# Performance work log

Measured on AMD Instinct MI355X. Metric: run time of the kernel, lower is better.

Reference implementation:

```python
import jax, jax.numpy as jnp
import numpy as np

N_EMB = 512
EMB_DIM = 64
DECAY = 0.99
EPS = 1e-5


def setup_inputs() -> dict:
    key = jax.random.key(0)
    k1, k2 = jax.random.split(key)
    x = jax.random.normal(k1, (32, EMB_DIM, 64, 64), dtype=jnp.float32)
    weight = jax.random.uniform(k2, (EMB_DIM, N_EMB), dtype=jnp.float32)  # rd_init=True: torch.rand(emb_dim, n_emb)
    cluster_size = jnp.zeros((N_EMB,), dtype=jnp.float32)
    embed_avg = weight  # buffer initialized as embed.clone()
    return {"x": x, "weight": weight, "cluster_size": cluster_size, "embed_avg": embed_avg}


def reference(x, weight, cluster_size, embed_avg):
    B, D, H, W = x.shape
    n_emb = weight.shape[1]
    # (B, D, H, W) -> (N, D) tokens
    flat = jnp.transpose(x, (0, 2, 3, 1)).reshape(-1, D)
    dist = (jnp.sum(flat * flat, axis=1, keepdims=True)
            - 2.0 * (flat @ weight)
            + jnp.sum(weight * weight, axis=0)[None, :])
    argmin = jnp.argmin(dist, axis=1)                      # (N,)
    quant = jnp.take(weight.T, argmin, axis=0)             # gather -> (N, D)
    result = jnp.transpose(quant.reshape(B, H, W, D), (0, 3, 1, 2))  # (B, D, H, W)

    # --- EMA codebook update (training branch) ---
    ones = jnp.ones(argmin.shape, dtype=x.dtype)
    n_idx = jax.ops.segment_sum(ones, argmin, num_segments=n_emb)    # onehot.sum(0)
    n_idx = jnp.where(n_idx == 0, jnp.ones_like(n_idx), n_idx)       # clamp empty clusters to 1
    new_cluster_size = DECAY * cluster_size + (1.0 - DECAY) * n_idx
    embed_sum = jax.ops.segment_sum(flat, argmin, num_segments=n_emb).T  # flatten.T @ onehot -> (D, n_emb)
    new_embed_avg = DECAY * embed_avg + (1.0 - DECAY) * embed_sum
    n = jnp.sum(new_cluster_size)
    cs = (new_cluster_size + EPS) / (n + n_emb * EPS) * n
    new_weight = new_embed_avg / cs[None, :]

    return result, argmin.reshape(B, H, W), new_weight, new_cluster_size, new_embed_avg
```

## Files before the change

kernel.cpp:

```cpp
#include <hip/hip_runtime.h>

#define NEMB 512
#define EMB 64
#define BSTR 262144
#define DECAYF 0.99f
#define OMDF 0.01f
#define EPSF 1e-5f
#define GAP_T 4e-4f
#define QCAP 32768

typedef __attribute__((ext_vector_type(8))) short bf16x8;
typedef __attribute__((ext_vector_type(4))) float f32x4;

__device__ __forceinline__ unsigned short f2bf(float f) {
    unsigned u = __float_as_uint(f);
    return (unsigned short)((u + 0x7FFFu + ((u >> 16) & 1u)) >> 16);
}
__device__ __forceinline__ float bf2f(unsigned short h) {
    return __uint_as_float(((unsigned)h) << 16);
}

__device__ __forceinline__ void gl2lds16(const void* g, void* l) {
    __builtin_amdgcn_global_load_lds(
        (const __attribute__((address_space(1))) unsigned int*)g,
        (__attribute__((address_space(3))) unsigned int*)l, 16, 0, 0);
}

__global__ void prep_kernel(const float* __restrict__ w,
                            unsigned short* __restrict__ wh, unsigned short* __restrict__ wl,
                            float* __restrict__ wsq,
                            float* __restrict__ cnt_ws, unsigned* __restrict__ gcnt) {
    int j = threadIdx.x;
    if (blockIdx.x < 8) {
        int d0 = blockIdx.x << 3;
        bf16x8 hb, lb;
#pragma unroll
        for (int i = 0; i < 8; ++i) {
            float v = w[(d0 + i) * NEMB + j];
            unsigned short h = f2bf(v);
            hb[i] = (short)h;
            lb[i] = (short)f2bf(v - bf2f(h));
        }
        *(bf16x8*)(wh + j * EMB + d0) = hb;
        *(bf16x8*)(wl + j * EMB + d0) = lb;
    } else {
        float s = 0.f;
#pragma unroll
        for (int d = 0; d < EMB; ++d) { float v = w[d * NEMB + j]; s = fmaf(v, v, s); }
        wsq[j] = s;
        cnt_ws[j] = 0.f;
        if (j == 0) *gcnt = 0u;
    }
}

#define UPD(S1, J1, S2, J2, s_, j_) do { \
    if (s_ < S1 || (s_ == S1 && j_ < J1)) { S2 = S1; J2 = J1; S1 = s_; J1 = j_; } \
    else if (s_ < S2 || (s_ == S2 && j_ < J2)) { S2 = s_; J2 = j_; } } while (0)

__global__ __launch_bounds__(512, 4) void vq_main(
    const float* __restrict__ x,
    const unsigned short* __restrict__ wh, const unsigned short* __restrict__ wl,
    const float* __restrict__ wsq,
    float* __restrict__ out_arg, unsigned* __restrict__ gcnt, int* __restrict__ queue)
{
    __shared__ __align__(16) unsigned char ubuf[32768];
    __shared__ float wsq_s[NEMB];

    float* xt = (float*)ubuf;
    unsigned short* whq = (unsigned short*)ubuf;
    unsigned short* wlq = whq + 8192;

    const int tid = threadIdx.x;
    const int blk = blockIdx.x;
    const int b    = blk >> 5;
    const int hgrp = blk & 31;
    const int t0 = b * 4096 + hgrp * 128;
    const float* xbase = x + b * BSTR + hgrp * 128;

    const int lane = tid & 63;
    const int wave = tid >> 6;

#pragma unroll
    for (int it = 0; it < 4; ++it) {
        int ch = wave + (it << 3);
        int d0 = ch << 1;
        gl2lds16(xbase + (d0 + (lane >> 5)) * 4096 + ((lane & 31) << 2),
                 xt + d0 * 128);
    }
    wsq_s[tid] = wsq[tid];
    __syncthreads();

    const int l15  = lane & 15;
    const int quad = lane >> 4;
    const int wbase = wave << 4;

    bf16x8 ah[2], al[2];
    float xq[4];
    {
        int m = wbase + l15;
        float sq = 0.f;
#pragma unroll
        for (int ks = 0; ks < 2; ++ks) {
            int k0 = (ks << 5) + (quad << 3);
            bf16x8 hh, ll;
#pragma unroll
            for (int i = 0; i < 8; ++i) {
                float v = xt[(k0 + i) * 128 + m];
                sq = fmaf(v, v, sq);
                unsigned short h = f2bf(v);
                hh[i] = (short)h;
                ll[i] = (short)f2bf(v - bf2f(h));
            }
            ah[ks] = hh; al[ks] = ll;
        }
        sq += __shfl_xor(sq, 16, 64);
        sq += __shfl_xor(sq, 32, 64);
#pragma unroll
        for (int r = 0; r < 4; ++r)
            xq[r] = __shfl(sq, (quad << 2) + r, 64);
    }
    __syncthreads();

    float v1[4], v2[4];
    int   j1[4];
#pragma unroll
    for (int r = 0; r < 4; ++r) { v1[r] = 3.4e38f; v2[r] = 3.4e38f; j1[r] = 0; }

    const int m7 = l15 & 7;
    const int s0off = ((quad ^ m7) << 3);
    const int s1off = (((4 | quad) ^ m7) << 3);

#pragma unroll
    for (int it = 0; it < 4; ++it) {
        int g0 = (wave << 6) + (it << 9);
        int arr = g0 >> 10;
        int win0 = g0 & 1023;
        int win = win0 + lane;
        int row = win >> 3, slot = win & 7;
        const unsigned short* src =
            (arr ? wl : wh) + row * EMB + ((slot ^ (row & 7)) << 3);
        gl2lds16(src, (arr ? wlq : whq) + (win0 << 3));
    }
    __syncthreads();

    for (int q = 0; q < 4; ++q) {
        const int nbase = q << 7;
#pragma unroll 2
        for (int it = 0; it < 8; ++it) {
            const int ib = ((it << 4) + l15) << 6;
            bf16x8 b0 = *(const bf16x8*)(whq + ib + s0off);
            bf16x8 b1 = *(const bf16x8*)(whq + ib + s1off);
            bf16x8 b2 = *(const bf16x8*)(wlq + ib + s0off);
            bf16x8 b3 = *(const bf16x8*)(wlq + ib + s1off);
            const int n = nbase + (it << 4) + l15;
            float wq = wsq_s[n];

            f32x4 acc = (f32x4){0.f, 0.f, 0.f, 0.f};
            acc = __builtin_amdgcn_mfma_f32_16x16x32_bf16(ah[0], b0, acc, 0, 0, 0);
            acc = __builtin_amdgcn_mfma_f32_16x16x32_bf16(ah[1], b1, acc, 0, 0, 0);
            acc = __builtin_amdgcn_mfma_f32_16x16x32_bf16(ah[0], b2, acc, 0, 0, 0);
            acc = __builtin_amdgcn_mfma_f32_16x16x32_bf16(ah[1], b3, acc, 0, 0, 0);
            acc = __builtin_amdgcn_mfma_f32_16x16x32_bf16(al[0], b0, acc, 0, 0, 0);
            acc = __builtin_amdgcn_mfma_f32_16x16x32_bf16(al[1], b1, acc, 0, 0, 0);
            acc = __builtin_amdgcn_mfma_f32_16x16x32_bf16(al[0], b2, acc, 0, 0, 0);
            acc = __builtin_amdgcn_mfma_f32_16x16x32_bf16(al[1], b3, acc, 0, 0, 0);

#pragma unroll
            for (int r = 0; r < 4; ++r) {
                float s0 = fmaf(-2.f, acc[r], xq[r] + wq);
                bool p0 = s0 < v1[r];
                float mx0 = fmaxf(s0, v1[r]);
                v1[r] = fminf(s0, v1[r]);
                v2[r] = fminf(v2[r], mx0);
                j1[r] = p0 ? n : j1[r];
            }
        }
        if (q < 3) {
            __syncthreads();
#pragma unroll
            for (int it = 0; it < 4; ++it) {
                int g0 = (wave << 6) + (it << 9);
                int arr = g0 >> 10;
                int win0 = g0 & 1023;
                int win = win0 + lane;
                int row = win >> 3, slot = win & 7;
                const unsigned short* src =
                    (arr ? wl : wh) + (((q + 1) << 7) + row) * EMB + ((slot ^ (row & 7)) << 3);
                gl2lds16(src, (arr ? wlq : whq) + (win0 << 3));
            }
            __syncthreads();
        }
    }

#pragma unroll
    for (int r = 0; r < 4; ++r) {
        float a1 = v1[r], a2 = v2[r];
        int   aj = j1[r];
#pragma unroll
        for (int msk = 1; msk < 16; msk <<= 1) {
            float o1 = __shfl_xor(a1, msk, 64);
            int   oj = __shfl_xor(aj, msk, 64);
            float o2 = __shfl_xor(a2, msk, 64);
            bool take = (o1 < a1) || (o1 == a1 && oj < aj);
            float mx = fmaxf(a1, o1);
            a2 = fminf(fminf(a2, o2), mx);
            a1 = fminf(a1, o1);
            aj = take ? oj : aj;
        }
        v1[r] = a1; v2[r] = a2; j1[r] = aj;
    }

    if (l15 == 0) {
#pragma unroll
        for (int r = 0; r < 4; ++r) {
            int gt = t0 + wbase + (quad << 2) + r;
            out_arg[gt] = (float)j1[r];
            if (v2[r] - v1[r] < GAP_T) {
                unsigned idx = atomicAdd(gcnt, 1u);
                if (idx < QCAP) queue[idx] = gt;
            }
        }
    }
}

__global__ __launch_bounds__(256) void refine_kernel(
    const float* __restrict__ x, const float* __restrict__ w,
    const float* __restrict__ wsq, const unsigned* __restrict__ gcnt,
    const int* __restrict__ queue, float* __restrict__ out_arg)
{
    __shared__ float wsq_s[NEMB];
    const int tid = threadIdx.x;
    wsq_s[tid] = wsq[tid];
    wsq_s[tid + 256] = wsq[tid + 256];
    __syncthreads();

    unsigned nfu = *gcnt;
    const int nf = (int)(nfu < (unsigned)QCAP ? nfu : (unsigned)QCAP);
    const int lane = tid & 63;
    const int gw = (blockIdx.x << 2) + (tid >> 6);

    for (int i = gw; i < nf; i += 1024) {
        const int t = queue[i] & 131071;
        const int b = t >> 12, pos = t & 4095;
        float xd = x[b * BSTR + lane * 4096 + pos];
        float xqv = xd * xd;
#pragma unroll
        for (int mk = 1; mk < 64; mk <<= 1) xqv += __shfl_xor(xqv, mk, 64);

        float accv[8];
#pragma unroll
        for (int k = 0; k < 8; ++k) accv[k] = 0.f;
#pragma unroll 4
        for (int d = 0; d < EMB; ++d) {
            float4 wa = *(const float4*)(w + d * NEMB + (lane << 2));
            float4 wb = *(const float4*)(w + d * NEMB + 256 + (lane << 2));
            float xv = __shfl(xd, d, 64);
            accv[0] = fmaf(xv, wa.x, accv[0]);
            accv[1] = fmaf(xv, wa.y, accv[1]);
            accv[2] = fmaf(xv, wa.z, accv[2]);
            accv[3] = fmaf(xv, wa.w, accv[3]);
            accv[4] = fmaf(xv, wb.x, accv[4]);
            accv[5] = fmaf(xv, wb.y, accv[5]);
            accv[6] = fmaf(xv, wb.z, accv[6]);
            accv[7] = fmaf(xv, wb.w, accv[7]);
        }

        float S1 = 3.4e38f, S2 = 3.4e38f; int J1 = 0, J2 = 0;
#pragma unroll
        for (int k = 0; k < 8; ++k) {
            int j = (k < 4) ? ((lane << 2) + k) : (256 + (lane << 2) + k - 4);
            float s = (xqv - 2.f * accv[k]) + wsq_s[j];
            UPD(S1, J1, S2, J2, s, j);
        }
#pragma unroll
        for (int mk = 1; mk < 64; mk <<= 1) {
            float os1 = __shfl_xor(S1, mk, 64); int oj1 = __shfl_xor(J1, mk, 64);
            float os2 = __shfl_xor(S2, mk, 64); int oj2 = __shfl_xor(J2, mk, 64);
            UPD(S1, J1, S2, J2, os1, oj1);
            UPD(S1, J1, S2, J2, os2, oj2);
        }

        int jm = J1;
        if (S2 - S1 < 1e-3f) {
            float w1 = w[lane * NEMB + J1];
            float w2 = w[lane * NEMB + J2];
            double e1 = (double)w1 * (double)w1 - 2.0 * (double)xd * (double)w1;
            double e2 = (double)w2 * (double)w2 - 2.0 * (double)xd * (double)w2;
#pragma unroll
            for (int mk = 1; mk < 64; mk <<= 1) {
                e1 += __shfl_xor(e1, mk, 64);
                e2 += __shfl_xor(e2, mk, 64);
            }
            if (e2 < e1 || (e2 == e1 && J2 < J1)) jm = J2;
        }
        if (lane == 0) out_arg[t] = (float)jm;
    }
}

__global__ __launch_bounds__(512, 4) void es_kernel(
    const float* __restrict__ x, const float* __restrict__ arg,
    float* __restrict__ es_p, float* __restrict__ cnt_ws)
{
    __shared__ unsigned short xh[16384];
    __shared__ int args_s[256];
    __shared__ float cacc[NEMB];

    const int tid = threadIdx.x;
    const int blk = blockIdx.x;
    const int flavor = blk & 1;
    const int chunk  = blk >> 1;
    const int b = chunk >> 3;
    const int tpos0 = (chunk & 7) << 9;

    cacc[tid] = 0.f;

    const int lane = tid & 63;
    const int wave = tid >> 6;
    const int l15  = lane & 15;
    const int quad = lane >> 4;
    const int jb   = wave << 5;

    f32x4 acc[4][2];
#pragma unroll
    for (int m = 0; m < 4; ++m)
#pragma unroll
        for (int nc = 0; nc < 2; ++nc) acc[m][nc] = (f32x4){0.f, 0.f, 0.f, 0.f};

    for (int st = 0; st < 2; ++st) {
        const int tpos = tpos0 + (st << 8);
#pragma unroll
        for (int it = 0; it < 8; ++it) {
            int idx = tid + (it << 9);
            int d = idx >> 6, q = idx & 63;
            float4 g = *(const float4*)(x + b * BSTR + d * 4096 + tpos + (q << 2));
            int c = q >> 1, half = q & 1;
            int off = d * 256 + ((c ^ (d & 7)) << 3) + (half << 2);
            ushort4 hv = {f2bf(g.x), f2bf(g.y), f2bf(g.z), f2bf(g.w)};
            *(ushort4*)(xh + off) = hv;
        }
        if (tid < 256) args_s[tid] = ((int)arg[b * 4096 + tpos + tid]) & 511;
        __syncthreads();

        if (flavor == 0 && tid < 256) atomicAdd(&cacc[args_s[tid]], 1.f);

#pragma unroll
        for (int kk = 0; kk < 8; ++kk) {
            bf16x8 a_[4];
#pragma unroll
            for (int m = 0; m < 4; ++m) {
                int d = (m << 4) + l15;
                int coff = ((((kk << 2) + quad) ^ (d & 7)) << 3);
                a_[m] = *(const bf16x8*)(xh + d * 256 + coff);
            }
            int argv[8];
            const int kb = (kk << 5) + (quad << 3);
#pragma unroll
            for (int i = 0; i < 8; ++i) argv[i] = args_s[kb + i];
#pragma unroll
            for (int nc = 0; nc < 2; ++nc) {
                const int jg = (flavor << 8) + jb + (nc << 4) + l15;
                bf16x8 bf;
#pragma unroll
                for (int i = 0; i < 8; ++i) bf[i] = (argv[i] == jg) ? (short)0x3F80 : (short)0;
#pragma unroll
                for (int m = 0; m < 4; ++m)
                    acc[m][nc] = __builtin_amdgcn_mfma_f32_16x16x32_bf16(a_[m], bf, acc[m][nc], 0, 0, 0);
            }
        }
        __syncthreads();
    }

    float* ep = es_p + blk * 16384;
#pragma unroll
    for (int m = 0; m < 4; ++m)
#pragma unroll
        for (int nc = 0; nc < 2; ++nc) {
            const int jl = jb + (nc << 4) + l15;
#pragma unroll
            for (int r = 0; r < 4; ++r) {
                const int d = (m << 4) + (quad << 2) + r;
                ep[d * 256 + jl] = acc[m][nc][r];
            }
        }
    if (flavor == 0) {
        float v = cacc[tid];
        if (v != 0.f) atomicAdd(&cnt_ws[tid], v);
    }
}

__global__ __launch_bounds__(256) void finalize_kernel(
    const float* __restrict__ cs_in, const float* __restrict__ avg_in,
    const float* __restrict__ cnt_ws, const float* __restrict__ es_p,
    float* __restrict__ out_w, float* __restrict__ out_ncs,
    float* __restrict__ out_avg) {
    __shared__ float red[256];
    const int tid = threadIdx.x;
    const int d  = blockIdx.x >> 1;
    const int jh = blockIdx.x & 1;

    float c0 = cnt_ws[tid], c1 = cnt_ws[tid + 256];
    float ncs0 = DECAYF * cs_in[tid] + OMDF * ((c0 == 0.f) ? 1.f : c0);
    float ncs1 = DECAYF * cs_in[tid + 256] + OMDF * ((c1 == 0.f) ? 1.f : c1);
    red[tid] = ncs0 + ncs1;
    __syncthreads();
    for (int s = 128; s > 0; s >>= 1) {
        if (tid < s) red[tid] += red[tid + s];
        __syncthreads();
    }
    const float n = red[0];

    const float* ep = es_p + jh * 16384 + d * 256 + tid;
    float s = 0.f;
#pragma unroll 16
    for (int c = 0; c < 256; ++c) s += ep[c * 32768];

    const float ncs = jh ? ncs1 : ncs0;
    const float csj = (ncs + EPSF) / (n + (float)NEMB * EPSF) * n;
    const int o = d * NEMB + (jh << 8) + tid;
    const float navg = DECAYF * avg_in[o] + OMDF * s;
    out_avg[o] = navg;
    out_w[o] = navg / csj;
    if (blockIdx.x == 0) { out_ncs[tid] = ncs0; out_ncs[tid + 256] = ncs1; }
}

__global__ __launch_bounds__(512) void result_kernel(
    const float* __restrict__ w, const float* __restrict__ arg,
    float* __restrict__ out_result)
{
    __shared__ float wrow8[8 * 512];
    const int tid = threadIdx.x;
    const int grp = blockIdx.x >> 6;
    const int chunk = blockIdx.x & 63;
#pragma unroll
    for (int d = 0; d < 8; ++d)
        wrow8[(d << 9) + tid] = w[((grp << 3) + d) * NEMB + tid];
    __syncthreads();

    const int t = (chunk << 11) + (tid << 2);
    const int o = (t >> 12) * BSTR + (t & 4095);
    float4 a4 = *(const float4*)(arg + t);
    int j0 = ((int)a4.x) & 511, j1 = ((int)a4.y) & 511;
    int j2 = ((int)a4.z) & 511, j3 = ((int)a4.w) & 511;
#pragma unroll
    for (int d = 0; d < 8; ++d) {
        const int dg = (grp << 3) + d;
        float4 r4 = {wrow8[(d << 9) + j0], wrow8[(d << 9) + j1],
                     wrow8[(d << 9) + j2], wrow8[(d << 9) + j3]};
        *(float4*)(out_result + o + dg * 4096) = r4;
    }
}

extern "C" void kernel_launch(void* const* d_in, const int* in_sizes, int n_in,
                              void* d_out, int out_size, void* d_ws, size_t ws_size,
                              hipStream_t stream) {
    (void)in_sizes; (void)n_in; (void)out_size; (void)ws_size;
    const float* x   = (const float*)d_in[0];
    const float* w   = (const float*)d_in[1];
    const float* cs  = (const float*)d_in[2];
    const float* avg = (const float*)d_in[3];

    float* out = (float*)d_out;
    float* out_result = out;
    float* out_arg    = out + 8388608;
    float* out_w      = out + 8519680;
    float* out_ncs    = out + 8552448;
    float* out_avg    = out + 8552960;
    float* es_p       = out;

    char* wsb = (char*)d_ws;
    unsigned short* wh = (unsigned short*)wsb;
    unsigned short* wl = (unsigned short*)(wsb + 65536);
    float* wsq      = (float*)(wsb + 131072);
    float* cnt_ws   = (float*)(wsb + 133120);
    unsigned* gcnt  = (unsigned*)(wsb + 135168);
    int* queue      = (int*)(wsb + 135232);

    prep_kernel<<<9, 512, 0, stream>>>(w, wh, wl, wsq, cnt_ws, gcnt);
    vq_main<<<1024, 512, 0, stream>>>(x, wh, wl, wsq, out_arg, gcnt, queue);
    refine_kernel<<<256, 256, 0, stream>>>(x, w, wsq, gcnt, queue, out_arg);
    es_kernel<<<512, 512, 0, stream>>>(x, out_arg, es_p, cnt_ws);
    finalize_kernel<<<128, 256, 0, stream>>>(cs, avg, cnt_ws, es_p, out_w, out_ncs, out_avg);
    result_kernel<<<512, 512, 0, stream>>>(w, out_arg, out_result);
}
```

Baseline: 178.5 us.

## Double-buffer codebook staging in LDS and drop low×low MFMA terms

Codebook staging changes from four sequential 128-entry chunks with a sync before and after each load to eight 64-entry chunks in two LDS slots. The next chunk is prefetched while the current one is consumed, so load latency overlaps MFMA work. The two lo×lo bf16 split MFMAs per tile are removed, cutting matrix work by a quarter at the cost of a small precision loss in the distance. The near-tie gap threshold is widened to compensate, which sends more tokens to the exact fallback queue.

```diff
diff --git a/kernel.cpp b/kernel.cpp
--- a/kernel.cpp
+++ b/kernel.cpp
@@ -6,7 +6,7 @@
 #define DECAYF 0.99f
 #define OMDF 0.01f
 #define EPSF 1e-5f
-#define GAP_T 4e-4f
+#define GAP_T 0.002f
 #define QCAP 32768
 
 typedef __attribute__((ext_vector_type(8))) short bf16x8;
@@ -57,6 +57,20 @@
     if (s_ < S1 || (s_ == S1 && j_ < J1)) { S2 = S1; J2 = J1; S1 = s_; J1 = j_; } \
     else if (s_ < S2 || (s_ == S2 && j_ < J2)) { S2 = s_; J2 = j_; } } while (0)
 
+#define STAGE_CB(slotk, cbase) do {                                               \
+    _Pragma("unroll")                                                             \
+    for (int it_ = 0; it_ < 2; ++it_) {                                           \
+        int win0_ = (wave << 6);                   \
+        int win_  = win0_ + lane;                                                 \
+        int row_  = win_ >> 3, sl_ = win_ & 7;                                    \
+        const unsigned short* src_ =                                              \
+            (it_ ? wl : wh) + ((cbase) + row_) * EMB + ((sl_ ^ (row_ & 7)) << 3); \
+        unsigned short* dst_ = (unsigned short*)ubuf + (slotk) * 8192             \
+                               + it_ * 4096 + (win0_ << 3);                       \
+        gl2lds16(src_, dst_);                                                     \
+    }                                                                             \
+} while (0)
+
 __global__ __launch_bounds__(512, 4) void vq_main(
     const float* __restrict__ x,
     const unsigned short* __restrict__ wh, const unsigned short* __restrict__ wl,
@@ -67,8 +81,6 @@
     __shared__ float wsq_s[NEMB];
 
     float* xt = (float*)ubuf;
-    unsigned short* whq = (unsigned short*)ubuf;
-    unsigned short* wlq = whq + 8192;
 
     const int tid = threadIdx.x;
     const int blk = blockIdx.x;
@@ -130,28 +142,22 @@
     const int s0off = ((quad ^ m7) << 3);
     const int s1off = (((4 | quad) ^ m7) << 3);
 
-#pragma unroll
-    for (int it = 0; it < 4; ++it) {
-        int g0 = (wave << 6) + (it << 9);
-        int arr = g0 >> 10;
-        int win0 = g0 & 1023;
-        int win = win0 + lane;
-        int row = win >> 3, slot = win & 7;
-        const unsigned short* src =
-            (arr ? wl : wh) + row * EMB + ((slot ^ (row & 7)) << 3);
-        gl2lds16(src, (arr ? wlq : whq) + (win0 << 3));
-    }
-    __syncthreads();
-
-    for (int q = 0; q < 4; ++q) {
-        const int nbase = q << 7;
-#pragma unroll 2
-        for (int it = 0; it < 8; ++it) {
+    STAGE_CB(0, 0);
+    __syncthreads();
+
+    for (int s = 0; s < 8; ++s) {
+        const int k = s & 1;
+        if (s < 7) STAGE_CB(k ^ 1, (s + 1) << 6);
+        const unsigned short* whs_k = (const unsigned short*)ubuf + k * 8192;
+        const unsigned short* wls_k = whs_k + 4096;
+        const int nbase = s << 6;
+#pragma unroll
+        for (int it = 0; it < 4; ++it) {
             const int ib = ((it << 4) + l15) << 6;
-            bf16x8 b0 = *(const bf16x8*)(whq + ib + s0off);
-            bf16x8 b1 = *(const bf16x8*)(whq + ib + s1off);
-            bf16x8 b2 = *(const bf16x8*)(wlq + ib + s0off);
-            bf16x8 b3 = *(const bf16x8*)(wlq + ib + s1off);
+            bf16x8 b0 = *(const bf16x8*)(whs_k + ib + s0off);
+            bf16x8 b1 = *(const bf16x8*)(whs_k + ib + s1off);
+            bf16x8 b2 = *(const bf16x8*)(wls_k + ib + s0off);
+            bf16x8 b3 = *(const bf16x8*)(wls_k + ib + s1off);
             const int n = nbase + (it << 4) + l15;
             float wq = wsq_s[n];
 
@@ -162,8 +168,6 @@
             acc = __builtin_amdgcn_mfma_f32_16x16x32_bf16(ah[1], b3, acc, 0, 0, 0);
             acc = __builtin_amdgcn_mfma_f32_16x16x32_bf16(al[0], b0, acc, 0, 0, 0);
             acc = __builtin_amdgcn_mfma_f32_16x16x32_bf16(al[1], b1, acc, 0, 0, 0);
-            acc = __builtin_amdgcn_mfma_f32_16x16x32_bf16(al[0], b2, acc, 0, 0, 0);
-            acc = __builtin_amdgcn_mfma_f32_16x16x32_bf16(al[1], b3, acc, 0, 0, 0);
 
 #pragma unroll
             for (int r = 0; r < 4; ++r) {
@@ -175,21 +179,7 @@
                 j1[r] = p0 ? n : j1[r];
             }
         }
-        if (q < 3) {
-            __syncthreads();
-#pragma unroll
-            for (int it = 0; it < 4; ++it) {
-                int g0 = (wave << 6) + (it << 9);
-                int arr = g0 >> 10;
-                int win0 = g0 & 1023;
-                int win = win0 + lane;
-                int row = win >> 3, slot = win & 7;
-                const unsigned short* src =
-                    (arr ? wl : wh) + (((q + 1) << 7) + row) * EMB + ((slot ^ (row & 7)) << 3);
-                gl2lds16(src, (arr ? wlq : whq) + (win0 << 3));
-            }
-            __syncthreads();
-        }
+        __syncthreads();
     }
 
 #pragma unroll
```

New measurement: 174.4 us. 1.02x faster.
